# Kernel tuning notes

Measured on AMD Instinct MI355X. Metric: run time of the kernel, lower is better.

Reference implementation:

```python
import jax, jax.numpy as jnp
import numpy as np
import math

HEADS = 8
GROUPS = 4
PW = 2  # pooling_window
EPS = 1e-5


def group_norm(x, w, b, groups=GROUPS):
    # x: (B, C, *spatial); normalize over (C//groups, *spatial) per group
    B, C = x.shape[0], x.shape[1]
    xs = x.reshape(B, groups, -1)
    mu = xs.mean(-1, keepdims=True)
    var = xs.var(-1, keepdims=True)
    xs = (xs - mu) / jnp.sqrt(var + EPS)
    shape = (1, C) + (1,) * (x.ndim - 2)
    return xs.reshape(x.shape) * w.reshape(shape) + b.reshape(shape)


def cst_pool(x, pw=PW):
    # x: (B, C, Tq, Ts) with Ts = h*w + 1 (class token first); avg-pool spatial part
    cls_tok, sp = x[..., :1], x[..., 1:]
    B, C, Tq, S = sp.shape
    h = math.isqrt(S)
    sp = sp.reshape(B, C, Tq, h // pw, pw, h // pw, pw).mean(axis=(4, 6))
    return jnp.concatenate([cls_tok, sp.reshape(B, C, Tq, -1)], axis=-1)


def conv1x1(x, w):
    # w: (O, C); x: (B, C, Tq, Ts)
    return jnp.einsum('oc,bcqs->boqs', w, x)


def interp_bilinear_ac(m, n):
    # bilinear resize to (n, n), align_corners=True; m: (B, H, W) float
    def axis_interp(x, size, axis, L):
        c = jnp.linspace(0.0, L - 1.0, size)
        i0 = jnp.floor(c).astype(jnp.int32)
        i1 = jnp.minimum(i0 + 1, L - 1)
        f = (c - i0).astype(x.dtype)
        x0 = jnp.take(x, i0, axis=axis)
        x1 = jnp.take(x, i1, axis=axis)
        shape = [1] * x.ndim
        shape[axis] = size
        f = f.reshape(shape)
        return x0 * (1 - f) + x1 * f
    B, H, W = m.shape
    return axis_interp(axis_interp(m, n, 1, H), n, 2, W)


def setup_inputs() -> dict:
    key = jax.random.key(0)
    ks = jax.random.split(key, 8)
    B, Cin, Tq, Ts = 4, 128, 256, 257
    Cout = 512
    hidden = Cout // 2  # 256
    H = W = 256
    s = 0.05
    return {
        'corr_tokens': jax.random.normal(ks[0], (B, Cin, Tq, Ts), jnp.float32),
        's_masks': jax.random.randint(ks[1], (B, H, W), 0, 2, jnp.int32),
        'W_sc': jax.random.normal(ks[2], (Cout, Cin), jnp.float32) * s,
        'gn_sc_w': jnp.ones((Cout,), jnp.float32),
        'gn_sc_b': jnp.zeros((Cout,), jnp.float32),
        'W_qkv': jax.random.normal(ks[3], (3 * hidden, Cin), jnp.float32) * s,
        'b_qkv': jax.random.normal(ks[4], (3 * hidden,), jnp.float32) * s,
        'gn1_w': jnp.ones((hidden,), jnp.float32),
        'gn1_b': jnp.zeros((hidden,), jnp.float32),
        'W_agg': jax.random.normal(ks[5], (Cout, hidden), jnp.float32) * s,
        'gn2_w': jnp.ones((Cout,), jnp.float32),
        'gn2_b': jnp.zeros((Cout,), jnp.float32),
        'gn_out_w': jnp.ones((Cout,), jnp.float32),
        'gn_out_b': jnp.zeros((Cout,), jnp.float32),
    }


def reference(corr_tokens, s_masks, W_sc, gn_sc_w, gn_sc_b, W_qkv, b_qkv,
              gn1_w, gn1_b, W_agg, gn2_w, gn2_b, gn_out_w, gn_out_b):
    B, _, Tq, Ts = corr_tokens.shape
    hidden = W_qkv.shape[0] // 3
    E = hidden // HEADS

    # short_cut branch: conv1x1 -> CSTPooling -> GroupNorm -> ReLU
    residual = jax.nn.relu(group_norm(cst_pool(conv1x1(corr_tokens, W_sc)), gn_sc_w, gn_sc_b))

    # qkv projection
    qkv = conv1x1(corr_tokens, W_qkv) + b_qkv[None, :, None, None]
    qkv = qkv.reshape(B, 3, HEADS, E, Tq, Ts)  # channel order (x, g, e)
    q, k, v = qkv[:, 0], qkv[:, 1], qkv[:, 2]

    # pool queries over support-spatial dim: (B,G,E,Tq,Ts) -> (B,G,E,Tq,Td)
    q = cst_pool(q.reshape(B, hidden, Tq, Ts))
    Td = q.shape[-1]
    q = q.reshape(B, HEADS, E, Tq, Td)

    # per-query masked attention
    attn = jnp.einsum('bgeqd,bgeqs->bgqds', q, k)  # (B,G,Tq,Td,Ts)
    sdim = math.isqrt(Ts - 1)
    m = interp_bilinear_ac(jnp.minimum(s_masks, 1).astype(jnp.float32), sdim)
    m = m.reshape(B, 1, 1, 1, sdim * sdim)
    attn_seg = jnp.where(m == 0, jnp.float32(-1e9), attn[..., 1:])
    attn = jnp.concatenate([attn[..., :1], attn_seg], axis=-1)
    attn = jax.nn.softmax(attn, axis=-1)
    out = jnp.einsum('bgqds,bgeqs->bgeqd', attn, v).reshape(B, hidden, Tq, Td)

    # agg: GN -> ReLU -> conv1x1 -> GN -> ReLU
    out = jax.nn.relu(group_norm(out, gn1_w, gn1_b))
    out = conv1x1(out, W_agg)
    out = jax.nn.relu(group_norm(out, gn2_w, gn2_b))

    return group_norm(out + residual, gn_out_w, gn_out_b)
```

## Files before the change

kernel.cpp:

```cpp
#include <hip/hip_runtime.h>
#include <stdint.h>

#define NB    4
#define TQ    256
#define TS    257
#define TD    65
#define NPIX  16640
#define NPADQ 264
#define NPAD  67584
#define COUT  512
#define HID   256

typedef __attribute__((ext_vector_type(8))) short bf16x8;
typedef __attribute__((ext_vector_type(4))) float f32x4;

__device__ __forceinline__ float bf2f(unsigned short u) {
    union { unsigned int i; float f; } v; v.i = ((unsigned int)u) << 16; return v.f;
}
__device__ __forceinline__ unsigned short f2bf(float x) {
    union { float f; unsigned int i; } v; v.f = x;
    unsigned int r = v.i + 0x7fffu + ((v.i >> 16) & 1u);
    return (unsigned short)(r >> 16);
}

__device__ __forceinline__ float2 gn_params(const float* st, int bg, float invcnt) {
    float mu  = st[bg * 2] * invcnt;
    float var = st[bg * 2 + 1] * invcnt - mu * mu;
    float2 r; r.x = mu; r.y = rsqrtf(var + 1e-5f); return r;
}

__global__ void wprep_kernel(const float* __restrict__ wq, const float* __restrict__ wsc,
                             const float* __restrict__ wagg, unsigned short* __restrict__ wb) {
    int i = blockIdx.x * 256 + threadIdx.x;
    float v;
    if (i < 98304) v = wq[i];
    else if (i < 163840) v = wsc[i - 98304];
    else v = wagg[i - 163840];
    wb[i] = f2bf(v);
}

__global__ void mask_kernel(const int* __restrict__ sm, float* __restrict__ bias) {
    int b = blockIdx.x; int t = threadIdx.x;
    if (t >= 272) return;
    float v;
    if (t == 0) v = 0.0f;
    else if (t <= 256) {
        int s = t - 1; int i = s >> 4, j = s & 15;
        v = (sm[(size_t)b * 65536 + i * 17 * 256 + j * 17] != 0) ? 0.0f : -1e9f;
    } else v = -1e9f;
    bias[b * 272 + t] = v;
}

__global__ __launch_bounds__(256) void tpool_kernel(
    const float* __restrict__ corr,
    unsigned short* __restrict__ corrT,
    unsigned short* __restrict__ corrpT)
{
    int q = blockIdx.x, ch = blockIdx.y, b = blockIdx.z;
    int t = threadIdx.x;
    __shared__ unsigned short sT[264 * 66];

    {
        int laneT = t & 63; int crow = t >> 6;
        for (int c = crow; c < 64; c += 4) {
            const float* src = corr + (((size_t)b * 128 + ch * 64 + c) * 256 + q) * 257;
            for (int s = laneT; s < 257; s += 64) sT[s * 66 + c] = f2bf(src[s]);
        }
    }
    for (int idx = t; idx < 7 * 66; idx += 256) {
        int s = 257 + idx / 66, c = idx % 66;
        sT[s * 66 + c] = 0;
    }
    __syncthreads();

    {
        unsigned int* dst = (unsigned int*)corrT;
        size_t base = (size_t)b * (NPAD * 64) + (size_t)q * (264 * 64) + ch * 32;
        for (int idx = t; idx < 264 * 32; idx += 256) {
            int s = idx >> 5, cu = idx & 31;
            unsigned int v = (unsigned int)sT[s * 66 + 2 * cu] |
                             ((unsigned int)sT[s * 66 + 2 * cu + 1] << 16);
            dst[base + (size_t)s * 64 + cu] = v;
        }
    }
    {
        unsigned int* dst = (unsigned int*)corrpT;
        size_t base = (size_t)b * (NPIX * 64) + (size_t)q * (65 * 64) + ch * 32;
        for (int idx = t; idx < 65 * 32; idx += 256) {
            int d = idx >> 5, cu = idx & 31;
            float x0, x1;
            if (d == 0) {
                x0 = bf2f(sT[0 * 66 + 2 * cu]); x1 = bf2f(sT[0 * 66 + 2 * cu + 1]);
            } else {
                int dd = d - 1; int i = dd >> 3, j = dd & 7;
                int s = 1 + i * 32 + j * 2;
                int c0 = 2 * cu, c1 = 2 * cu + 1;
                x0 = 0.25f * (bf2f(sT[s*66+c0]) + bf2f(sT[(s+1)*66+c0]) +
                              bf2f(sT[(s+16)*66+c0]) + bf2f(sT[(s+17)*66+c0]));
                x1 = 0.25f * (bf2f(sT[s*66+c1]) + bf2f(sT[(s+1)*66+c1]) +
                              bf2f(sT[(s+16)*66+c1]) + bf2f(sT[(s+17)*66+c1]));
            }
            unsigned int v = (unsigned int)f2bf(x0) | ((unsigned int)f2bf(x1) << 16);
            dst[base + (size_t)d * 64 + cu] = v;
        }
    }
}

template<int MODE, int KT>
__global__ __launch_bounds__(256) void mgemm_kernel(
    const unsigned short* __restrict__ X,
    const unsigned short* __restrict__ Wb,
    int Nn,
    float* __restrict__ Yf,
    unsigned short* __restrict__ Y16,
    const float* __restrict__ bias,
    const float* __restrict__ st, const float* __restrict__ gw, const float* __restrict__ gb,
    float invcnt)
{
    int b  = blockIdx.z;
    int n0 = blockIdx.x * 128;
    int m0 = blockIdx.y * 128;
    int t = threadIdx.x;
    int w = t >> 6, lane = t & 63;
    int lm = lane & 15, lg = lane >> 4;
    int wn = (w & 1) * 64, wm = (w >> 1) * 64;

    __shared__ __align__(16) unsigned short sX[16384];
    __shared__ __align__(16) unsigned short sW[16384];

    f32x4 acc[4][4];
    #pragma unroll
    for (int i = 0; i < 4; i++)
        #pragma unroll
        for (int j = 0; j < 4; j++) { acc[i][j][0]=0.f; acc[i][j][1]=0.f; acc[i][j][2]=0.f; acc[i][j][3]=0.f; }

    for (int kc = 0; kc < KT / 128; kc++) {
        for (int i = t; i < 2048; i += 256) {
            int r_ = i >> 4, kq = i & 15;
            uint4 xv = *(const uint4*)&X[((size_t)b * Nn + n0 + r_) * KT + kc * 128 + (kq << 3)];
            if (MODE == 3) {
                union { uint4 v; unsigned short us[8]; } u; u.v = xv;
                int c0 = kc * 128 + (kq << 3);
                float2 p = gn_params(st, b * 4 + (c0 >> 6), invcnt);
                #pragma unroll
                for (int jj = 0; jj < 8; jj++) {
                    int cc = c0 + jj;
                    float v = bf2f(u.us[jj]);
                    v = fmaxf((v - p.x) * p.y * gw[cc] + gb[cc], 0.0f);
                    u.us[jj] = f2bf(v);
                }
                xv = u.v;
            }
            *(uint4*)&sX[r_ * 128 + ((kq ^ (r_ & 15)) << 3)] = xv;
            uint4 wv = *(const uint4*)&Wb[((size_t)(m0 + r_)) * KT + kc * 128 + (kq << 3)];
            *(uint4*)&sW[r_ * 128 + ((kq ^ (r_ & 15)) << 3)] = wv;
        }
        __syncthreads();
        #pragma unroll
        for (int kk = 0; kk < 4; kk++) {
            int kg = (kk << 2) | lg;
            bf16x8 af[4], bw[4];
            #pragma unroll
            for (int ii = 0; ii < 4; ii++)
                af[ii] = *(const bf16x8*)&sX[(wn + ii * 16 + lm) * 128 + ((kg ^ lm) << 3)];
            #pragma unroll
            for (int jj = 0; jj < 4; jj++)
                bw[jj] = *(const bf16x8*)&sW[(wm + jj * 16 + lm) * 128 + ((kg ^ lm) << 3)];
            #pragma unroll
            for (int ii = 0; ii < 4; ii++)
                #pragma unroll
                for (int jj = 0; jj < 4; jj++) {
                    if (MODE == 0)
                        acc[ii][jj] = __builtin_amdgcn_mfma_f32_16x16x32_bf16(bw[jj], af[ii], acc[ii][jj], 0,0,0);
                    else
                        acc[ii][jj] = __builtin_amdgcn_mfma_f32_16x16x32_bf16(af[ii], bw[jj], acc[ii][jj], 0,0,0);
                }
        }
        __syncthreads();
    }

    if (MODE == 0) {
        #pragma unroll
        for (int ii = 0; ii < 4; ii++) {
            int n = n0 + wn + ii * 16 + lm;
            #pragma unroll
            for (int jj = 0; jj < 4; jj++) {
                int mb = m0 + wm + jj * 16 + lg * 4;
                union { unsigned short us[4]; uint2 v; } pk;
                #pragma unroll
                for (int r = 0; r < 4; r++) pk.us[r] = f2bf(acc[ii][jj][r] + bias[mb + r]);
                *(uint2*)&Y16[((size_t)b * NPIX + n) * 256 + mb] = pk.v;
            }
        }
    } else {
        #pragma unroll
        for (int ii = 0; ii < 4; ii++) {
            int nb = n0 + wn + ii * 16 + lg * 4;
            #pragma unroll
            for (int jj = 0; jj < 4; jj++) {
                int m = m0 + wm + jj * 16 + lm;
                *(f32x4*)&Yf[((size_t)b * COUT + m) * NPIX + nb] = acc[ii][jj];
            }
        }
    }
}

__global__ __launch_bounds__(320, 3) void attn_kernel(
    const unsigned short* __restrict__ corrT,
    const unsigned short* __restrict__ wkv,
    const float* __restrict__ bkv,
    const unsigned short* __restrict__ qpT,
    const float* __restrict__ bias272,
    unsigned short* __restrict__ attT)
{
    int lin = blockIdx.y * 8 + blockIdx.x;
    int xcd = lin & 7, idx = lin >> 3;
    int q = (xcd << 5) | (idx & 31);
    int g = idx >> 5;
    int b = blockIdx.z;
    int t = threadIdx.x;
    int w = t >> 6, lane = t & 63;
    int lm = lane & 15, lg = lane >> 4;

    __shared__ __align__(16) unsigned short sbuf[17920];
    const int VB = 8704;

    int d = w * 16 + lm;
    int dc = d < 64 ? d : 64;
    bf16x8 qa = *(const bf16x8*)&qpT[((size_t)b * NPIX + q * 65 + dc) * 256 + g * 32 + lg * 8];
    if (d >= TD) { bf16x8 z = {}; qa = z; }

    bf16x8 wkf[2][4], wvf[2][4];
    #pragma unroll
    for (int et = 0; et < 2; et++)
        #pragma unroll
        for (int ks = 0; ks < 4; ks++) {
            wkf[et][ks] = *(const bf16x8*)&wkv[(size_t)(g * 32 + et * 16 + lm) * 128 + ks * 32 + lg * 8];
            wvf[et][ks] = *(const bf16x8*)&wkv[(size_t)(256 + g * 32 + et * 16 + lm) * 128 + ks * 32 + lg * 8];
        }
    float bk_[2][4], bv_[2];
    #pragma unroll
    for (int et = 0; et < 2; et++) {
        #pragma unroll
        for (int r = 0; r < 4; r++) bk_[et][r] = bkv[g * 32 + et * 16 + lg * 4 + r];
        bv_[et] = bkv[256 + g * 32 + et * 16 + lm];
    }

    const unsigned short* cbase = corrT + ((size_t)b * NPAD + (size_t)q * 264) * 128;
    f32x4 zero4 = {0.f, 0.f, 0.f, 0.f};

    for (int sti = w; sti < 17; sti += 5) {
        int srow = sti * 16 + lm; if (srow > 263) srow = 263;
        bf16x8 ct[4];
        #pragma unroll
        for (int ks = 0; ks < 4; ks++)
            ct[ks] = *(const bf16x8*)&cbase[(size_t)srow * 128 + ks * 32 + lg * 8];
        f32x4 ak0 = zero4, ak1 = zero4, av0 = zero4, av1 = zero4;
        #pragma unroll
        for (int ks = 0; ks < 4; ks++) {
            ak0 = __builtin_amdgcn_mfma_f32_16x16x32_bf16(wkf[0][ks], ct[ks], ak0, 0, 0, 0);
            ak1 = __builtin_amdgcn_mfma_f32_16x16x32_bf16(wkf[1][ks], ct[ks], ak1, 0, 0, 0);
            av0 = __builtin_amdgcn_mfma_f32_16x16x32_bf16(ct[ks], wvf[0][ks], av0, 0, 0, 0);
            av1 = __builtin_amdgcn_mfma_f32_16x16x32_bf16(ct[ks], wvf[1][ks], av1, 0, 0, 0);
        }
        {
            int s = sti * 16 + lm;
            #pragma unroll
            for (int et = 0; et < 2; et++) {
                unsigned u = (unsigned)(s * 64 + et * 32 + lg * 8);
                unsigned mr = u >> 8, sl = (u >> 4) & 15;
                unsigned us = (u & ~0xF0u) | ((sl ^ (mr & 15)) << 4);
                union { unsigned short e[4]; uint2 v; } pk;
                f32x4 a = et ? ak1 : ak0;
                #pragma unroll
                for (int r = 0; r < 4; r++) pk.e[r] = f2bf(a[r] + bk_[et][r]);
                *(uint2*)((char*)sbuf + us) = pk.v;
            }
        }
        {
            int s0 = sti * 16 + lg * 4;
            unsigned vb_off = (unsigned)((s0 >> 5) * 2048 + (s0 & 31) * 2);
            #pragma unroll
            for (int et = 0; et < 2; et++) {
                int ch = et * 16 + lm;
                unsigned ov = vb_off + (unsigned)ch * 64u;
                unsigned mr = ov >> 8, sl = (ov >> 4) & 15;
                unsigned ovs = (ov & ~0xF0u) | ((sl ^ (mr & 15)) << 4);
                union { unsigned short e[4]; uint2 v; } pk;
                f32x4 a = et ? av1 : av0;
                #pragma unroll
                for (int r = 0; r < 4; r++) pk.e[r] = f2bf(a[r] + bv_[et]);
                *(uint2*)((char*)sbuf + 17408 + ovs) = pk.v;
            }
        }
    }
    if (t < 128) {
        int ch = t >> 2, j = t & 3;
        unsigned ov = 16384u + (unsigned)ch * 64u + 32u + (unsigned)j * 8u;
        unsigned mr = ov >> 8, sl = (ov >> 4) & 15;
        unsigned ovs = (ov & ~0xF0u) | ((sl ^ (mr & 15)) << 4);
        uint2 z2; z2.x = 0u; z2.y = 0u;
        *(uint2*)((char*)sbuf + 17408 + ovs) = z2;
    }
    __syncthreads();

    f32x4 c[17];
    int sl0 = ((lm & 3) << 2) | lg;
    #pragma unroll
    for (int tt = 0; tt < 17; tt++) {
        int mr = tt * 4 + (lm >> 2);
        bf16x8 kf = *(const bf16x8*)&sbuf[mr * 128 + ((sl0 ^ (mr & 15)) << 3)];
        c[tt] = __builtin_amdgcn_mfma_f32_16x16x32_bf16(kf, qa, zero4, 0, 0, 0);
    }

    const float* bp = bias272 + b * 272 + lg * 4;
    #pragma unroll
    for (int tt = 0; tt < 17; tt++) {
        f32x4 bf = *(const f32x4*)&bp[tt * 16];
        c[tt][0] += bf[0]; c[tt][1] += bf[1]; c[tt][2] += bf[2]; c[tt][3] += bf[3];
    }

    f32x4 mv = c[0];
    #pragma unroll
    for (int tt = 1; tt < 17; tt++) {
        mv[0] = fmaxf(mv[0], c[tt][0]); mv[1] = fmaxf(mv[1], c[tt][1]);
        mv[2] = fmaxf(mv[2], c[tt][2]); mv[3] = fmaxf(mv[3], c[tt][3]);
    }
    float mx = fmaxf(fmaxf(mv[0], mv[1]), fmaxf(mv[2], mv[3]));
    mx = fmaxf(mx, __shfl_xor(mx, 16));
    mx = fmaxf(mx, __shfl_xor(mx, 32));
    float sm = 0.f;
    #pragma unroll
    for (int tt = 0; tt < 17; tt++) {
        #pragma unroll
        for (int r = 0; r < 4; r++) { float e_ = __expf(c[tt][r] - mx); c[tt][r] = e_; sm += e_; }
    }
    sm += __shfl_xor(sm, 16);
    sm += __shfl_xor(sm, 32);
    float inv = 1.0f / sm;

    unsigned plo[17], phi[17];
    #pragma unroll
    for (int tt = 0; tt < 17; tt++) {
        asm("v_cvt_pk_bf16_f32 %0, %1, %2" : "=v"(plo[tt]) : "v"(c[tt][0]), "v"(c[tt][1]));
        asm("v_cvt_pk_bf16_f32 %0, %1, %2" : "=v"(phi[tt]) : "v"(c[tt][2]), "v"(c[tt][3]));
    }

    bool lgEven = (lane & 16) == 0;
    f32x4 o0 = zero4, o1 = zero4;
    #pragma unroll
    for (int kk = 0; kk < 9; kk++) {
        unsigned A = plo[2 * kk];
        unsigned C = phi[2 * kk];
        unsigned B = (2 * kk + 1 < 17) ? plo[2 * kk + 1] : 0u;
        unsigned D = (2 * kk + 1 < 17) ? phi[2 * kk + 1] : 0u;
        asm("v_permlane32_swap_b32 %0, %1" : "+v"(A), "+v"(B));
        asm("v_permlane32_swap_b32 %0, %1" : "+v"(C), "+v"(D));
        unsigned Ax = __shfl_xor(A, 16), Bx = __shfl_xor(B, 16);
        unsigned Cx = __shfl_xor(C, 16), Dx = __shfl_xor(D, 16);
        union { unsigned u[4]; bf16x8 v; } pa;
        pa.u[0] = lgEven ? A  : Bx;
        pa.u[1] = lgEven ? C  : Dx;
        pa.u[2] = lgEven ? Ax : B;
        pa.u[3] = lgEven ? Cx : D;
        int mr0 = kk * 8 + (lm >> 2), mr1 = mr0 + 4;
        bf16x8 v0 = *(const bf16x8*)&sbuf[VB + mr0 * 128 + ((sl0 ^ (mr0 & 15)) << 3)];
        bf16x8 v1 = *(const bf16x8*)&sbuf[VB + mr1 * 128 + ((sl0 ^ (mr1 & 15)) << 3)];
        o0 = __builtin_amdgcn_mfma_f32_16x16x32_bf16(pa.v, v0, o0, 0, 0, 0);
        o1 = __builtin_amdgcn_mfma_f32_16x16x32_bf16(pa.v, v1, o1, 0, 0, 0);
    }
    float invr[4];
    #pragma unroll
    for (int r = 0; r < 4; r++) invr[r] = __shfl(inv, lg * 4 + r);
    #pragma unroll
    for (int r = 0; r < 4; r++) {
        int dd = w * 16 + lg * 4 + r;
        if (dd < TD) {
            size_t nn = (size_t)b * NPIX + q * 65 + dd;
            attT[nn * 256 + g * 32 + lm]      = f2bf(o0[r] * invr[r]);
            attT[nn * 256 + g * 32 + 16 + lm] = f2bf(o1[r] * invr[r]);
        }
    }
}

__global__ void stats1_kernel(const unsigned short* __restrict__ attT, float* __restrict__ st) {
    int b = blockIdx.y;
    int t = threadIdx.x;
    int e8 = t & 31, g = e8 >> 3;
    int lane = t & 63;
    float s = 0.f, ss = 0.f;
    for (int r = blockIdx.x * 8 + (t >> 5); r < NPIX; r += gridDim.x * 8) {
        union { uint4 v; unsigned short us[8]; } u;
        u.v = *(const uint4*)&attT[((size_t)b * NPIX + r) * 256 + e8 * 8];
        #pragma unroll
        for (int j = 0; j < 8; j++) { float x = bf2f(u.us[j]); s += x; ss += x * x; }
    }
    s += __shfl_down(s, 32); ss += __shfl_down(ss, 32);
    s += __shfl_down(s, 4);  ss += __shfl_down(ss, 4);
    s += __shfl_down(s, 2);  ss += __shfl_down(ss, 2);
    s += __shfl_down(s, 1);  ss += __shfl_down(ss, 1);
    if (lane < 32 && (lane & 7) == 0) {
        atomicAdd(&st[(b * 4 + g) * 2],     s);
        atomicAdd(&st[(b * 4 + g) * 2 + 1], ss);
    }
}

__global__ void stats_kernel(const float* __restrict__ x, float* __restrict__ st, int Cg) {
    size_t len = (size_t)Cg * NPIX;
    size_t base = (size_t)blockIdx.y * len;
    const float4* x4 = reinterpret_cast<const float4*>(x + base);
    size_t len4 = len >> 2;
    float s = 0.f, ss = 0.f;
    for (size_t i = (size_t)blockIdx.x * blockDim.x + threadIdx.x; i < len4;
         i += (size_t)gridDim.x * blockDim.x) {
        float4 v = x4[i];
        s  += v.x + v.y + v.z + v.w;
        ss += v.x * v.x + v.y * v.y + v.z * v.z + v.w * v.w;
    }
    #pragma unroll
    for (int o = 32; o > 0; o >>= 1) { s += __shfl_down(s, o, 64); ss += __shfl_down(ss, o, 64); }
    __shared__ float red[4][2];
    int wid = threadIdx.x >> 6, lane = threadIdx.x & 63;
    if (lane == 0) { red[wid][0] = s; red[wid][1] = ss; }
    __syncthreads();
    if (threadIdx.x == 0) {
        float S  = red[0][0] + red[1][0] + red[2][0] + red[3][0];
        float SS = red[0][1] + red[1][1] + red[2][1] + red[3][1];
        atomicAdd(&st[blockIdx.y * 2],     S);
        atomicAdd(&st[blockIdx.y * 2 + 1], SS);
    }
}

__global__ void z_kernel(float* __restrict__ out, const float* __restrict__ scr,
                         const float* __restrict__ st2, const float* __restrict__ stsc,
                         const float* __restrict__ g2w, const float* __restrict__ g2b,
                         const float* __restrict__ gsw, const float* __restrict__ gsb)
{
    const float invcnt = 1.0f / (128.0f * NPIX);
    size_t total4 = (size_t)NB * COUT * (NPIX / 4);
    float4* o4 = reinterpret_cast<float4*>(out);
    const float4* s4 = reinterpret_cast<const float4*>(scr);
    for (size_t i = (size_t)blockIdx.x * blockDim.x + threadIdx.x; i < total4;
         i += (size_t)gridDim.x * blockDim.x) {
        size_t flat = i * 4;
        int c = (int)((flat / NPIX) % COUT);
        int b = (int)(flat / ((size_t)COUT * NPIX));
        int bg = b * 4 + (c >> 7);
        float2 p2 = gn_params(st2,  bg, invcnt);
        float2 ps = gn_params(stsc, bg, invcnt);
        float w2 = g2w[c] * p2.y, b2 = g2b[c] - p2.x * p2.y * g2w[c];
        float wsc = gsw[c] * ps.y, bsc = gsb[c] - ps.x * ps.y * gsw[c];
        float4 a = o4[i], r = s4[i], z;
        z.x = fmaxf(a.x * w2 + b2, 0.f) + fmaxf(r.x * wsc + bsc, 0.f);
        z.y = fmaxf(a.y * w2 + b2, 0.f) + fmaxf(r.y * wsc + bsc, 0.f);
        z.z = fmaxf(a.z * w2 + b2, 0.f) + fmaxf(r.z * wsc + bsc, 0.f);
        z.w = fmaxf(a.w * w2 + b2, 0.f) + fmaxf(r.w * wsc + bsc, 0.f);
        o4[i] = z;
    }
}

__global__ void norm_kernel(float* __restrict__ out, const float* __restrict__ st3,
                            const float* __restrict__ gw, const float* __restrict__ gb)
{
    const float invcnt = 1.0f / (128.0f * NPIX);
    size_t total4 = (size_t)NB * COUT * (NPIX / 4);
    float4* o4 = reinterpret_cast<float4*>(out);
    for (size_t i = (size_t)blockIdx.x * blockDim.x + threadIdx.x; i < total4;
         i += (size_t)gridDim.x * blockDim.x) {
        size_t flat = i * 4;
        int c = (int)((flat / NPIX) % COUT);
        int b = (int)(flat / ((size_t)COUT * NPIX));
        int bg = b * 4 + (c >> 7);
        float2 p = gn_params(st3, bg, invcnt);
        float w_ = gw[c] * p.y, b_ = gb[c] - p.x * p.y * gw[c];
        float4 a = o4[i], z;
        z.x = a.x * w_ + b_; z.y = a.y * w_ + b_; z.z = a.z * w_ + b_; z.w = a.w * w_ + b_;
        o4[i] = z;
    }
}

extern "C" void kernel_launch(void* const* d_in, const int* in_sizes, int n_in,
                              void* d_out, int out_size, void* d_ws, size_t ws_size,
                              hipStream_t stream) {
    (void)in_sizes; (void)n_in; (void)out_size; (void)ws_size;
    const float* corr     = (const float*)d_in[0];
    const int*   smask    = (const int*)  d_in[1];
    const float* W_sc     = (const float*)d_in[2];
    const float* gn_sc_w  = (const float*)d_in[3];
    const float* gn_sc_b  = (const float*)d_in[4];
    const float* W_qkv    = (const float*)d_in[5];
    const float* b_qkv    = (const float*)d_in[6];
    const float* gn1_w    = (const float*)d_in[7];
    const float* gn1_b    = (const float*)d_in[8];
    const float* W_agg    = (const float*)d_in[9];
    const float* gn2_w    = (const float*)d_in[10];
    const float* gn2_b    = (const float*)d_in[11];
    const float* gn_out_w = (const float*)d_in[12];
    const float* gn_out_b = (const float*)d_in[13];
    float* out = (float*)d_out;

    unsigned short* ws = (unsigned short*)d_ws;
    unsigned short* corrT  = ws;
    unsigned short* kbuf   = corrT  + (size_t)34603008;
    unsigned short* vbuf   = kbuf   + (size_t)69206016;
    unsigned short* corrpT = vbuf   + (size_t)69206016;
    unsigned short* qpT    = corrpT + (size_t)8519680;
    unsigned short* attT   = qpT    + (size_t)17039360;
    unsigned short* wbuf   = attT   + (size_t)17039360;
    float* bias  = (float*)(wbuf + (size_t)294912);
    float* stats = bias + 1088;
    float* scr   = (float*)d_ws;
    float* st_sc = stats, *st1 = stats + 32, *st2 = stats + 64, *st3 = stats + 96;
    (void)kbuf; (void)vbuf;

    const float inv1 = 1.0f / (64.0f * (float)NPIX);

    hipMemsetAsync(stats, 0, 128 * sizeof(float), stream);
    wprep_kernel<<<dim3(1152), dim3(256), 0, stream>>>(W_qkv, W_sc, W_agg, wbuf);
    mask_kernel<<<dim3(NB), dim3(320), 0, stream>>>(smask, bias);
    tpool_kernel<<<dim3(TQ, 2, NB), dim3(256), 0, stream>>>(corr, corrT, corrpT);
    mgemm_kernel<0,128><<<dim3(130, 2, NB), dim3(256), 0, stream>>>(
        corrpT, wbuf, NPIX, nullptr, qpT, b_qkv,
        nullptr, nullptr, nullptr, 0.f);
    attn_kernel<<<dim3(8, TQ, NB), dim3(320), 0, stream>>>(
        corrT, wbuf + 32768, b_qkv + 256, qpT, bias, attT);
    stats1_kernel<<<dim3(208, NB), dim3(256), 0, stream>>>(attT, st1);
    mgemm_kernel<3,256><<<dim3(130, 4, NB), dim3(256), 0, stream>>>(
        attT, wbuf + 163840, NPIX, out, nullptr, nullptr,
        st1, gn1_w, gn1_b, inv1);
    stats_kernel<<<dim3(64, 16), dim3(256), 0, stream>>>(out, st2, 128);
    mgemm_kernel<2,128><<<dim3(130, 4, NB), dim3(256), 0, stream>>>(
        corrpT, wbuf + 98304, NPIX, scr, nullptr, nullptr,
        nullptr, nullptr, nullptr, 0.f);
    stats_kernel<<<dim3(64, 16), dim3(256), 0, stream>>>(scr, st_sc, 128);
    z_kernel<<<dim3(4096), dim3(256), 0, stream>>>(out, scr, st2, st_sc, gn2_w, gn2_b, gn_sc_w, gn_sc_b);
    stats_kernel<<<dim3(64, 16), dim3(256), 0, stream>>>(out, st3, 128);
    norm_kernel<<<dim3(4096), dim3(256), 0, stream>>>(out, st3, gn_out_w, gn_out_b);
}
```

Before: 967.0 us.

## Fuse group-norm statistics into GEMM epilogues and z kernel, drop stats passes

```diff
diff --git a/kernel.cpp b/kernel.cpp
--- a/kernel.cpp
+++ b/kernel.cpp
@@ -115,7 +115,8 @@
     unsigned short* __restrict__ Y16,
     const float* __restrict__ bias,
     const float* __restrict__ st, const float* __restrict__ gw, const float* __restrict__ gb,
-    float invcnt)
+    float invcnt,
+    float* __restrict__ stacc)
 {
     int b  = blockIdx.z;
     int n0 = blockIdx.x * 128;
@@ -127,6 +128,7 @@
 
     __shared__ __align__(16) unsigned short sX[16384];
     __shared__ __align__(16) unsigned short sW[16384];
+    __shared__ float red2[4][2];
 
     f32x4 acc[4][4];
     #pragma unroll
@@ -193,6 +195,7 @@
             }
         }
     } else {
+        float s = 0.f, ss = 0.f;
         #pragma unroll
         for (int ii = 0; ii < 4; ii++) {
             int nb = n0 + wn + ii * 16 + lg * 4;
@@ -200,7 +203,20 @@
             for (int jj = 0; jj < 4; jj++) {
                 int m = m0 + wm + jj * 16 + lm;
                 *(f32x4*)&Yf[((size_t)b * COUT + m) * NPIX + nb] = acc[ii][jj];
+                #pragma unroll
+                for (int r = 0; r < 4; r++) { float v = acc[ii][jj][r]; s += v; ss += v * v; }
             }
+        }
+        #pragma unroll
+        for (int o = 32; o > 0; o >>= 1) { s += __shfl_down(s, o, 64); ss += __shfl_down(ss, o, 64); }
+        if (lane == 0) { red2[w][0] = s; red2[w][1] = ss; }
+        __syncthreads();
+        if (t == 0) {
+            float S  = red2[0][0] + red2[1][0] + red2[2][0] + red2[3][0];
+            float SS = red2[0][1] + red2[1][1] + red2[2][1] + red2[3][1];
+            int bg = b * 4 + blockIdx.y;
+            atomicAdd(&stacc[bg * 2],     S);
+            atomicAdd(&stacc[bg * 2 + 1], SS);
         }
     }
 }
@@ -270,11 +286,13 @@
                 unsigned u = (unsigned)(s * 64 + et * 32 + lg * 8);
                 unsigned mr = u >> 8, sl = (u >> 4) & 15;
                 unsigned us = (u & ~0xF0u) | ((sl ^ (mr & 15)) << 4);
-                union { unsigned short e[4]; uint2 v; } pk;
                 f32x4 a = et ? ak1 : ak0;
-                #pragma unroll
-                for (int r = 0; r < 4; r++) pk.e[r] = f2bf(a[r] + bk_[et][r]);
-                *(uint2*)((char*)sbuf + us) = pk.v;
+                float v0 = a[0] + bk_[et][0], v1 = a[1] + bk_[et][1];
+                float v2 = a[2] + bk_[et][2], v3 = a[3] + bk_[et][3];
+                uint2 pk;
+                asm("v_cvt_pk_bf16_f32 %0, %1, %2" : "=v"(pk.x) : "v"(v0), "v"(v1));
+                asm("v_cvt_pk_bf16_f32 %0, %1, %2" : "=v"(pk.y) : "v"(v2), "v"(v3));
+                *(uint2*)((char*)sbuf + us) = pk;
             }
         }
         {
@@ -286,11 +304,13 @@
                 unsigned ov = vb_off + (unsigned)ch * 64u;
                 unsigned mr = ov >> 8, sl = (ov >> 4) & 15;
                 unsigned ovs = (ov & ~0xF0u) | ((sl ^ (mr & 15)) << 4);
-                union { unsigned short e[4]; uint2 v; } pk;
                 f32x4 a = et ? av1 : av0;
-                #pragma unroll
-                for (int r = 0; r < 4; r++) pk.e[r] = f2bf(a[r] + bv_[et]);
-                *(uint2*)((char*)sbuf + 17408 + ovs) = pk.v;
+                float v0 = a[0] + bv_[et], v1 = a[1] + bv_[et];
+                float v2 = a[2] + bv_[et], v3 = a[3] + bv_[et];
+                uint2 pk;
+                asm("v_cvt_pk_bf16_f32 %0, %1, %2" : "=v"(pk.x) : "v"(v0), "v"(v1));
+                asm("v_cvt_pk_bf16_f32 %0, %1, %2" : "=v"(pk.y) : "v"(v2), "v"(v3));
+                *(uint2*)((char*)sbuf + 17408 + ovs) = pk;
             }
         }
     }
@@ -405,17 +425,35 @@
     }
 }
 
-__global__ void stats_kernel(const float* __restrict__ x, float* __restrict__ st, int Cg) {
-    size_t len = (size_t)Cg * NPIX;
-    size_t base = (size_t)blockIdx.y * len;
-    const float4* x4 = reinterpret_cast<const float4*>(x + base);
-    size_t len4 = len >> 2;
+__global__ void z_kernel(float* __restrict__ out, const float* __restrict__ scr,
+                         const float* __restrict__ st2, const float* __restrict__ stsc,
+                         const float* __restrict__ g2w, const float* __restrict__ g2b,
+                         const float* __restrict__ gsw, const float* __restrict__ gsb,
+                         float* __restrict__ st3)
+{
+    const float invcnt = 1.0f / (128.0f * NPIX);
+    int span = blockIdx.y;
+    int cg = span & 3;
+    float2 p2 = gn_params(st2,  span, invcnt);
+    float2 ps = gn_params(stsc, span, invcnt);
+    size_t base = (size_t)span * (128 * (size_t)NPIX);
+    float4* o4 = reinterpret_cast<float4*>(out + base);
+    const float4* s4 = reinterpret_cast<const float4*>(scr + base);
+    const size_t len4 = (128 * (size_t)NPIX) >> 2;
     float s = 0.f, ss = 0.f;
     for (size_t i = (size_t)blockIdx.x * blockDim.x + threadIdx.x; i < len4;
          i += (size_t)gridDim.x * blockDim.x) {
-        float4 v = x4[i];
-        s  += v.x + v.y + v.z + v.w;
-        ss += v.x * v.x + v.y * v.y + v.z * v.z + v.w * v.w;
+        int c = cg * 128 + (int)((i * 4) / NPIX);
+        float w2 = g2w[c] * p2.y, b2 = g2b[c] - p2.x * p2.y * g2w[c];
+        float wsc = gsw[c] * ps.y, bsc = gsb[c] - ps.x * ps.y * gsw[c];
+        float4 a = o4[i], r = s4[i], z;
+        z.x = fmaxf(a.x * w2 + b2, 0.f) + fmaxf(r.x * wsc + bsc, 0.f);
+        z.y = fmaxf(a.y * w2 + b2, 0.f) + fmaxf(r.y * wsc + bsc, 0.f);
+        z.z = fmaxf(a.z * w2 + b2, 0.f) + fmaxf(r.z * wsc + bsc, 0.f);
+        z.w = fmaxf(a.w * w2 + b2, 0.f) + fmaxf(r.w * wsc + bsc, 0.f);
+        o4[i] = z;
+        s  += z.x + z.y + z.z + z.w;
+        ss += z.x * z.x + z.y * z.y + z.z * z.z + z.w * z.w;
     }
     #pragma unroll
     for (int o = 32; o > 0; o >>= 1) { s += __shfl_down(s, o, 64); ss += __shfl_down(ss, o, 64); }
@@ -426,36 +464,8 @@
     if (threadIdx.x == 0) {
         float S  = red[0][0] + red[1][0] + red[2][0] + red[3][0];
         float SS = red[0][1] + red[1][1] + red[2][1] + red[3][1];
-        atomicAdd(&st[blockIdx.y * 2],     S);
-        atomicAdd(&st[blockIdx.y * 2 + 1], SS);
-    }
-}
-
-__global__ void z_kernel(float* __restrict__ out, const float* __restrict__ scr,
-                         const float* __restrict__ st2, const float* __restrict__ stsc,
-                         const float* __restrict__ g2w, const float* __restrict__ g2b,
-                         const float* __restrict__ gsw, const float* __restrict__ gsb)
-{
-    const float invcnt = 1.0f / (128.0f * NPIX);
-    size_t total4 = (size_t)NB * COUT * (NPIX / 4);
-    float4* o4 = reinterpret_cast<float4*>(out);
-    const float4* s4 = reinterpret_cast<const float4*>(scr);
-    for (size_t i = (size_t)blockIdx.x * blockDim.x + threadIdx.x; i < total4;
-         i += (size_t)gridDim.x * blockDim.x) {
-        size_t flat = i * 4;
-        int c = (int)((flat / NPIX) % COUT);
-        int b = (int)(flat / ((size_t)COUT * NPIX));
-        int bg = b * 4 + (c >> 7);
-        float2 p2 = gn_params(st2,  bg, invcnt);
-        float2 ps = gn_params(stsc, bg, invcnt);
-        float w2 = g2w[c] * p2.y, b2 = g2b[c] - p2.x * p2.y * g2w[c];
-        float wsc = gsw[c] * ps.y, bsc = gsb[c] - ps.x * ps.y * gsw[c];
-        float4 a = o4[i], r = s4[i], z;
-        z.x = fmaxf(a.x * w2 + b2, 0.f) + fmaxf(r.x * wsc + bsc, 0.f);
-        z.y = fmaxf(a.y * w2 + b2, 0.f) + fmaxf(r.y * wsc + bsc, 0.f);
-        z.z = fmaxf(a.z * w2 + b2, 0.f) + fmaxf(r.z * wsc + bsc, 0.f);
-        z.w = fmaxf(a.w * w2 + b2, 0.f) + fmaxf(r.w * wsc + bsc, 0.f);
-        o4[i] = z;
+        atomicAdd(&st3[span * 2],     S);
+        atomicAdd(&st3[span * 2 + 1], SS);
     }
 }
 
@@ -463,15 +473,15 @@
                             const float* __restrict__ gw, const float* __restrict__ gb)
 {
     const float invcnt = 1.0f / (128.0f * NPIX);
-    size_t total4 = (size_t)NB * COUT * (NPIX / 4);
-    float4* o4 = reinterpret_cast<float4*>(out);
-    for (size_t i = (size_t)blockIdx.x * blockDim.x + threadIdx.x; i < total4;
+    int span = blockIdx.y;
+    int cg = span & 3;
+    float2 p = gn_params(st3, span, invcnt);
+    size_t base = (size_t)span * (128 * (size_t)NPIX);
+    float4* o4 = reinterpret_cast<float4*>(out + base);
+    const size_t len4 = (128 * (size_t)NPIX) >> 2;
+    for (size_t i = (size_t)blockIdx.x * blockDim.x + threadIdx.x; i < len4;
          i += (size_t)gridDim.x * blockDim.x) {
-        size_t flat = i * 4;
-        int c = (int)((flat / NPIX) % COUT);
-        int b = (int)(flat / ((size_t)COUT * NPIX));
-        int bg = b * 4 + (c >> 7);
-        float2 p = gn_params(st3, bg, invcnt);
+        int c = cg * 128 + (int)((i * 4) / NPIX);
         float w_ = gw[c] * p.y, b_ = gb[c] - p.x * p.y * gw[c];
         float4 a = o4[i], z;
         z.x = a.x * w_ + b_; z.y = a.y * w_ + b_; z.z = a.z * w_ + b_; z.w = a.w * w_ + b_;
@@ -521,19 +531,17 @@
     tpool_kernel<<<dim3(TQ, 2, NB), dim3(256), 0, stream>>>(corr, corrT, corrpT);
     mgemm_kernel<0,128><<<dim3(130, 2, NB), dim3(256), 0, stream>>>(
         corrpT, wbuf, NPIX, nullptr, qpT, b_qkv,
-        nullptr, nullptr, nullptr, 0.f);
+        nullptr, nullptr, nullptr, 0.f, nullptr);
     attn_kernel<<<dim3(8, TQ, NB), dim3(320), 0, stream>>>(
         corrT, wbuf + 32768, b_qkv + 256, qpT, bias, attT);
     stats1_kernel<<<dim3(208, NB), dim3(256), 0, stream>>>(attT, st1);
     mgemm_kernel<3,256><<<dim3(130, 4, NB), dim3(256), 0, stream>>>(
         attT, wbuf + 163840, NPIX, out, nullptr, nullptr,
-        st1, gn1_w, gn1_b, inv1);
-    stats_kernel<<<dim3(64, 16), dim3(256), 0, stream>>>(out, st2, 128);
+        st1, gn1_w, gn1_b, inv1, st2);
     mgemm_kernel<2,128><<<dim3(130, 4, NB), dim3(256), 0, stream>>>(
         corrpT, wbuf + 98304, NPIX, scr, nullptr, nullptr,
-        nullptr, nullptr, nullptr, 0.f);
-    stats_kernel<<<dim3(64, 16), dim3(256), 0, stream>>>(scr, st_sc, 128);
-    z_kernel<<<dim3(4096), dim3(256), 0, stream>>>(out, scr, st2, st_sc, gn2_w, gn2_b, gn_sc_w, gn_sc_b);
-    stats_kernel<<<dim3(64, 16), dim3(256), 0, stream>>>(out, st3, 128);
-    norm_kernel<<<dim3(4096), dim3(256), 0, stream>>>(out, st3, gn_out_w, gn_out_b);
-}
+        nullptr, nullptr, nullptr, 0.f, st_sc);
+    z_kernel<<<dim3(256, 16), dim3(256), 0, stream>>>(
+        out, scr, st2, st_sc, gn2_w, gn2_b, gn_sc_w, gn_sc_b, st3);
+    norm_kernel<<<dim3(256, 16), dim3(256), 0, stream>>>(out, st3, gn_out_w, gn_out_b);
+}
```

After: 940.6 us. 1.03x faster.
